# Kernel tuning notes

Measured on AMD Instinct MI355X. Metric: run time of the kernel, lower is better.

Reference implementation:

```python
import jax, jax.numpy as jnp
import numpy as np
import math

IN_DIM = 256
HID_DIM = 256
NUM_EDGE_TYPES = 3
HEADS = 8
HEAD_DIM = HID_DIM // HEADS  # 32
QK_DIM = (NUM_EDGE_TYPES + 1) * HID_DIM  # 1024
N = 4096


def _glorot(key, shape):
    # torch_geometric-style glorot: uniform(-a, a), a = sqrt(6/(fan_in+fan_out)) over last two dims
    a = math.sqrt(6.0 / (shape[-2] + shape[-1]))
    return jax.random.uniform(key, shape, jnp.float32, -a, a)


def setup_inputs() -> dict:
    key = jax.random.key(0)
    ks = jax.random.split(key, 8)
    return {
        "input_x": jax.random.normal(ks[0], (N, IN_DIM), jnp.float32),
        "pe_Q": jax.random.normal(ks[1], (N, NUM_EDGE_TYPES * HID_DIM), jnp.float32),
        "pe_K": jax.random.normal(ks[2], (N, NUM_EDGE_TYPES * HID_DIM), jnp.float32),
        "A": jnp.zeros((N, N), jnp.int32),  # accepted by forward but unused
        "WQ": _glorot(ks[3], (HEADS, QK_DIM, HEAD_DIM)),
        "WK": _glorot(ks[4], (HEADS, QK_DIM, HEAD_DIM)),
        "WV": _glorot(ks[5], (HEADS, IN_DIM, HEAD_DIM)),
        "Q_bias": jnp.zeros((HEADS, 1, HEAD_DIM), jnp.float32),
        "K_bias": jnp.zeros((HEADS, 1, HEAD_DIM), jnp.float32),
        "V_bias": jnp.zeros((HEADS, 1, HEAD_DIM), jnp.float32),
        "lin_w": _glorot(ks[6], (HID_DIM, HID_DIM)),
        "lin_b": jnp.zeros((HID_DIM,), jnp.float32),
    }


def reference(input_x, pe_Q, pe_K, A, WQ, WK, WV, Q_bias, K_bias, V_bias, lin_w, lin_b):
    x_Q = jnp.concatenate([input_x, pe_Q], axis=-1)  # [N, QK_DIM]
    x_K = jnp.concatenate([input_x, pe_K], axis=-1)  # [N, QK_DIM]
    Q = jnp.einsum('nd,hdk->hnk', x_Q, WQ) + Q_bias   # [H, N, hd]
    K = jnp.einsum('nd,hdk->hnk', x_K, WK) + K_bias   # [H, N, hd]
    V = jnp.einsum('nd,hdk->hnk', input_x, WV) + V_bias
    scores = jnp.einsum('hnk,hmk->hnm', Q, K) / math.sqrt(HID_DIM)  # [H, N, N]
    scores = scores - jax.lax.stop_gradient(jnp.max(scores, axis=-1, keepdims=True))
    attn = jax.nn.softmax(scores, axis=-1)
    attn = jnp.where(jnp.isnan(attn), jnp.zeros_like(attn), attn)
    attn_x = jnp.einsum('hnm,hmk->hnk', attn, V)      # [H, N, hd]
    # cat(list over heads, dim=1) -> [N, H*hd] with head-major column order
    x_cat = jnp.transpose(attn_x, (1, 0, 2)).reshape(attn_x.shape[1], -1)
    return x_cat @ lin_w.T + lin_b
```

## Files before the change

kernel.cpp:

```cpp
#include <hip/hip_runtime.h>
#include <hip/hip_bf16.h>

typedef __attribute__((ext_vector_type(8))) short bf16x8;
typedef __attribute__((ext_vector_type(4))) float f32x4;

#define QSCALE 0.09016844f

__device__ __forceinline__ unsigned short f2b(float f) {
    union { float f; unsigned int u; } v; v.f = f;
    unsigned int u = v.u;
    unsigned int r = (u + 0x7FFFu + ((u >> 16) & 1u)) >> 16;
    return (unsigned short)r;
}
__device__ __forceinline__ float b2f(unsigned short h) {
    union { unsigned int u; float f; } v; v.u = ((unsigned int)h) << 16;
    return v.f;
}
__device__ __forceinline__ unsigned pk2(float a, float b) {
    union { __hip_bfloat162 h; unsigned u; } c;
    c.h = __float22bfloat162_rn(make_float2(a, b));
    return c.u;
}

__global__ __launch_bounds__(256) void prep_main(
    const float* __restrict__ WQ, const float* __restrict__ WK,
    const float* __restrict__ WV, const float* __restrict__ LW,
    const float* __restrict__ Qb, const float* __restrict__ Kb,
    const float* __restrict__ Vb,
    const float* __restrict__ x, const float* __restrict__ peQ,
    const float* __restrict__ peK,
    unsigned short* __restrict__ WQt, unsigned short* __restrict__ WKt,
    unsigned short* __restrict__ WVt, unsigned short* __restrict__ LWt,
    unsigned short* __restrict__ Bq, unsigned short* __restrict__ Bk,
    unsigned short* __restrict__ Bv,
    unsigned short* __restrict__ xb, unsigned short* __restrict__ peQb,
    unsigned short* __restrict__ peKb) {
    int b = blockIdx.x, t = threadIdx.x;
    if (b < 288) {
        const float* W; unsigned short* Wt; int h, d0, D; float sc = 1.0f;
        if (b < 128)      { W = WQ; Wt = WQt; h = b >> 4;   d0 = (b & 15) * 64; D = 1024; sc = QSCALE; }
        else if (b < 256) { int bb = b - 128; W = WK; Wt = WKt; h = bb >> 4; d0 = (bb & 15) * 64; D = 1024; }
        else              { int bb = b - 256; W = WV; Wt = WVt; h = bb >> 2; d0 = (bb & 3) * 64;  D = 256; }
        __shared__ float Ts[32][65];
        int dr = t >> 2, k0 = (t & 3) * 8;
        const float* src = W + (h * D + d0 + dr) * 32 + k0;
        float4 u0 = *(const float4*)src;
        float4 u1 = *(const float4*)(src + 4);
        Ts[k0 + 0][dr] = u0.x; Ts[k0 + 1][dr] = u0.y; Ts[k0 + 2][dr] = u0.z; Ts[k0 + 3][dr] = u0.w;
        Ts[k0 + 4][dr] = u1.x; Ts[k0 + 5][dr] = u1.y; Ts[k0 + 6][dr] = u1.z; Ts[k0 + 7][dr] = u1.w;
        __syncthreads();
        int k = t >> 3, dc = (t & 7) * 8;
        union { unsigned short s[8]; uint4 v; } pk;
#pragma unroll
        for (int i = 0; i < 8; i++) pk.s[i] = f2b(Ts[k][dc + i] * sc);
        *(uint4*)(Wt + (h * 32 + k) * D + d0 + dc) = pk.v;
    } else if (b < 320) {
        int base = (b - 288) * 2048 + t * 8;
        const float* sp = LW + base;
        float4 u0 = *(const float4*)sp;
        float4 u1 = *(const float4*)(sp + 4);
        union { unsigned u[4]; uint4 v; } pk;
        pk.u[0] = pk2(u0.x, u0.y); pk.u[1] = pk2(u0.z, u0.w);
        pk.u[2] = pk2(u1.x, u1.y); pk.u[3] = pk2(u1.z, u1.w);
        *(uint4*)(LWt + base) = pk.v;
    } else if (b == 320) {
        Bq[t] = f2b(Qb[t] * QSCALE); Bk[t] = f2b(Kb[t]); Bv[t] = f2b(Vb[t]);
    } else {
        int idx = (b - 321) * 2048 + t * 8;
        const float* sp; unsigned short* dp;
        if (idx < 1048576)      { sp = x + idx;                dp = xb + idx; }
        else if (idx < 4194304) { sp = peQ + (idx - 1048576);  dp = peQb + (idx - 1048576); }
        else                    { sp = peK + (idx - 4194304);  dp = peKb + (idx - 4194304); }
        float4 u0 = *(const float4*)sp;
        float4 u1 = *(const float4*)(sp + 4);
        union { unsigned u[4]; uint4 v; } pk;
        pk.u[0] = pk2(u0.x, u0.y); pk.u[1] = pk2(u0.z, u0.w);
        pk.u[2] = pk2(u1.x, u1.y); pk.u[3] = pk2(u1.z, u1.w);
        *(uint4*)dp = pk.v;
    }
}

__global__ __launch_bounds__(256) void prep_fb(
    const float* __restrict__ WQ, const float* __restrict__ WK,
    const float* __restrict__ WV,
    const float* __restrict__ Qb, const float* __restrict__ Kb,
    const float* __restrict__ Vb,
    unsigned short* __restrict__ WQt, unsigned short* __restrict__ WKt,
    unsigned short* __restrict__ WVt,
    unsigned short* __restrict__ Bq, unsigned short* __restrict__ Bk,
    unsigned short* __restrict__ Bv) {
    int b = blockIdx.x, t = threadIdx.x;
    if (b < 288) {
        const float* W; unsigned short* Wt; int h, d0, D; float sc = 1.0f;
        if (b < 128)      { W = WQ; Wt = WQt; h = b >> 4;   d0 = (b & 15) * 64; D = 1024; sc = QSCALE; }
        else if (b < 256) { int bb = b - 128; W = WK; Wt = WKt; h = bb >> 4; d0 = (bb & 15) * 64; D = 1024; }
        else              { int bb = b - 256; W = WV; Wt = WVt; h = bb >> 2; d0 = (bb & 3) * 64;  D = 256; }
        __shared__ float Ts[32][65];
        int dr = t >> 2, k0 = (t & 3) * 8;
        const float* src = W + (h * D + d0 + dr) * 32 + k0;
        float4 u0 = *(const float4*)src;
        float4 u1 = *(const float4*)(src + 4);
        Ts[k0 + 0][dr] = u0.x; Ts[k0 + 1][dr] = u0.y; Ts[k0 + 2][dr] = u0.z; Ts[k0 + 3][dr] = u0.w;
        Ts[k0 + 4][dr] = u1.x; Ts[k0 + 5][dr] = u1.y; Ts[k0 + 6][dr] = u1.z; Ts[k0 + 7][dr] = u1.w;
        __syncthreads();
        int k = t >> 3, dc = (t & 7) * 8;
        union { unsigned short s[8]; uint4 v; } pk;
#pragma unroll
        for (int i = 0; i < 8; i++) pk.s[i] = f2b(Ts[k][dc + i] * sc);
        *(uint4*)(Wt + (h * 32 + k) * D + d0 + dc) = pk.v;
    } else {
        Bq[t] = f2b(Qb[t] * QSCALE); Bk[t] = f2b(Kb[t]); Bv[t] = f2b(Vb[t]);
    }
}

template <bool ABF16>
__global__ __launch_bounds__(256) void proj_fused(
    const void* __restrict__ xv,
    const void* __restrict__ peQv, const void* __restrict__ peKv,
    const unsigned short* __restrict__ WQt, const unsigned short* __restrict__ WKt,
    const unsigned short* __restrict__ WVt,
    const unsigned short* __restrict__ Bq, const unsigned short* __restrict__ Bk,
    const unsigned short* __restrict__ Bv,
    unsigned short* __restrict__ Qc, unsigned short* __restrict__ KV) {
    __shared__ unsigned short As[64 * 72];
    __shared__ unsigned short Bs[64 * 72];
    int bx = blockIdx.x;
    int which = bx >> 8, bb = bx & 255;
    const void* A1; const unsigned short* Bt; const unsigned short* bias; int K;
    if (which == 0)      { A1 = peQv; Bt = WQt; bias = Bq; K = 1024; }
    else if (which == 1) { A1 = peKv; Bt = WKt; bias = Bk; K = 1024; }
    else                 { A1 = peQv; Bt = WVt; bias = Bv; K = 256; }
    int mb = bb & 63, nb = bb >> 6;
    int m0 = mb * 64, n0 = nb * 64;
    int t = threadIdx.x, w = t >> 6, lane = t & 63;
    int ln = lane & 15, q8 = (lane >> 4) * 8;
    int wm = (w >> 1) * 32, wn = (w & 1) * 32;
    int sr = t >> 3, sc = (t & 7) * 8;
    f32x4 acc[2][2];
#pragma unroll
    for (int i = 0; i < 2; i++)
#pragma unroll
        for (int j = 0; j < 2; j++) acc[i][j] = (f32x4){0.f, 0.f, 0.f, 0.f};
    for (int kb = 0; kb < K; kb += 64) {
#pragma unroll
        for (int half = 0; half < 2; half++) {
            int r = sr + half * 32;
            int c = kb + sc;
            if (ABF16) {
                const unsigned short* ap = (c < 256)
                    ? ((const unsigned short*)xv + (m0 + r) * 256 + c)
                    : ((const unsigned short*)A1 + (m0 + r) * 768 + (c - 256));
                *(uint4*)&As[r * 72 + sc] = *(const uint4*)ap;
            } else {
                const float* ap = (c < 256)
                    ? ((const float*)xv + (m0 + r) * 256 + c)
                    : ((const float*)A1 + (m0 + r) * 768 + (c - 256));
                float4 u0 = *(const float4*)ap;
                float4 u1 = *(const float4*)(ap + 4);
                union { unsigned u[4]; uint4 v; } pk;
                pk.u[0] = pk2(u0.x, u0.y); pk.u[1] = pk2(u0.z, u0.w);
                pk.u[2] = pk2(u1.x, u1.y); pk.u[3] = pk2(u1.z, u1.w);
                *(uint4*)&As[r * 72 + sc] = pk.v;
            }
            *(uint4*)&Bs[r * 72 + sc] = *(const uint4*)(Bt + (n0 + r) * K + c);
        }
        __syncthreads();
#pragma unroll
        for (int ks = 0; ks < 64; ks += 32) {
            bf16x8 a[2], b[2];
#pragma unroll
            for (int i = 0; i < 2; i++) {
                a[i] = *(const bf16x8*)&As[(wm + i * 16 + ln) * 72 + ks + q8];
                b[i] = *(const bf16x8*)&Bs[(wn + i * 16 + ln) * 72 + ks + q8];
            }
#pragma unroll
            for (int i = 0; i < 2; i++)
#pragma unroll
                for (int j = 0; j < 2; j++)
                    acc[i][j] = __builtin_amdgcn_mfma_f32_16x16x32_bf16(a[i], b[j], acc[i][j], 0, 0, 0);
        }
        __syncthreads();
    }
#pragma unroll
    for (int j = 0; j < 2; j++) {
        int ncol = n0 + wn + j * 16 + ln;
        float bv = b2f(bias[ncol]);
        int h2 = ncol >> 5, din = ncol & 31;
#pragma unroll
        for (int i = 0; i < 2; i++) {
            int rbase = m0 + wm + i * 16 + ((lane >> 4) * 4);
            if (which == 0) {
#pragma unroll
                for (int r = 0; r < 4; r++)
                    Qc[(rbase + r) * 256 + ncol] = f2b(acc[i][j][r] + bv);
            } else if (which == 1) {
#pragma unroll
                for (int r = 0; r < 4; r++) {
                    int key = rbase + r;
                    int T2 = key >> 6, k6 = key & 63;
                    int kt = ((k6 >> 2) & 1) + ((k6 >> 4) & 2);
                    int ln2 = ((k6 >> 3) & 3) * 4 + (k6 & 3);
                    int addr = (h2 * 64 + T2) * 4096 + kt * 512
                             + ((din >> 3) * 16 + ln2) * 8 + (din & 7);
                    KV[addr] = f2b(acc[i][j][r] + bv);
                }
            } else {
                int key = rbase;
                int T2 = key >> 6, k6 = key & 63;
                int chunk = 4 + ((din >> 4) << 1) + ((k6 >> 5) & 1);
                int lane2 = ((k6 >> 3) & 3) * 16 + (din & 15);
                int addr = (h2 * 64 + T2) * 4096 + chunk * 512 + lane2 * 8 + (k6 & 7);
                uint2 vv;
                vv.x = pk2(acc[i][j][0] + bv, acc[i][j][1] + bv);
                vv.y = pk2(acc[i][j][2] + bv, acc[i][j][3] + bv);
                *(uint2*)(KV + addr) = vv;
            }
        }
    }
}

__global__ __launch_bounds__(512, 4) void attn_kernel(
    const unsigned short* __restrict__ Qc,
    const unsigned short* __restrict__ KV,
    unsigned short* __restrict__ Xc) {
    __shared__ float Om[8][32][33];
    __shared__ float Ls[8][32];
    int head = blockIdx.x & 7;
    int qb = blockIdx.x >> 3;
    int t = threadIdx.x, w = t >> 6, lane = t & 63;
    int ln = lane & 15, quad = lane >> 4, q8 = quad * 8;
    int wq = w >> 2, wk = w & 3;
    int q0 = qb * 64;
    bf16x8 qfv[2];
#pragma unroll
    for (int qf = 0; qf < 2; qf++)
        qfv[qf] = *(const bf16x8*)(Qc + (q0 + wq * 32 + qf * 16 + ln) * 256 + head * 32 + q8);
    const unsigned short* kv = KV + (head * 64 + wk * 16) * 4096 + lane * 8;
    f32x4 o[2][2];
    float lts[2] = {0.f, 0.f};
#pragma unroll
    for (int qf = 0; qf < 2; qf++)
#pragma unroll
        for (int hh = 0; hh < 2; hh++) o[qf][hh] = (f32x4){0.f, 0.f, 0.f, 0.f};
    const f32x4 z = {0.f, 0.f, 0.f, 0.f};
    bf16x8 k0 = *(const bf16x8*)(kv + 0);
    bf16x8 k1 = *(const bf16x8*)(kv + 512);
    bf16x8 k2 = *(const bf16x8*)(kv + 1024);
    bf16x8 k3 = *(const bf16x8*)(kv + 1536);
    bf16x8 v0 = *(const bf16x8*)(kv + 2048);
    bf16x8 v1 = *(const bf16x8*)(kv + 2560);
    bf16x8 v2 = *(const bf16x8*)(kv + 3072);
    bf16x8 v3 = *(const bf16x8*)(kv + 3584);
#pragma unroll 1
    for (int it = 0; it < 16; it++) {
        int nit = (it < 15) ? (it + 1) : 15;
        const unsigned short* nkv = kv + nit * 4096;
        bf16x8 nk0 = *(const bf16x8*)(nkv + 0);
        bf16x8 nk1 = *(const bf16x8*)(nkv + 512);
        bf16x8 nk2 = *(const bf16x8*)(nkv + 1024);
        bf16x8 nk3 = *(const bf16x8*)(nkv + 1536);
        bf16x8 nv0 = *(const bf16x8*)(nkv + 2048);
        bf16x8 nv1 = *(const bf16x8*)(nkv + 2560);
        bf16x8 nv2 = *(const bf16x8*)(nkv + 3072);
        bf16x8 nv3 = *(const bf16x8*)(nkv + 3584);
#pragma unroll
        for (int qf = 0; qf < 2; qf++) {
            f32x4 s0 = __builtin_amdgcn_mfma_f32_16x16x32_bf16(k0, qfv[qf], z, 0, 0, 0);
            f32x4 s1 = __builtin_amdgcn_mfma_f32_16x16x32_bf16(k1, qfv[qf], z, 0, 0, 0);
            f32x4 s2 = __builtin_amdgcn_mfma_f32_16x16x32_bf16(k2, qfv[qf], z, 0, 0, 0);
            f32x4 s3 = __builtin_amdgcn_mfma_f32_16x16x32_bf16(k3, qfv[qf], z, 0, 0, 0);
            float p0[4], p1[4], p2[4], p3[4];
#pragma unroll
            for (int r = 0; r < 4; r++) {
                p0[r] = __builtin_amdgcn_exp2f(s0[r]);
                p1[r] = __builtin_amdgcn_exp2f(s1[r]);
                p2[r] = __builtin_amdgcn_exp2f(s2[r]);
                p3[r] = __builtin_amdgcn_exp2f(s3[r]);
            }
            float psum = 0.f;
#pragma unroll
            for (int r = 0; r < 4; r++) psum += (p0[r] + p1[r]) + (p2[r] + p3[r]);
            lts[qf] += psum;
            union { unsigned u[4]; bf16x8 v; } b0, b1;
            b0.u[0] = pk2(p0[0], p0[1]); b0.u[1] = pk2(p0[2], p0[3]);
            b0.u[2] = pk2(p1[0], p1[1]); b0.u[3] = pk2(p1[2], p1[3]);
            b1.u[0] = pk2(p2[0], p2[1]); b1.u[1] = pk2(p2[2], p2[3]);
            b1.u[2] = pk2(p3[0], p3[1]); b1.u[3] = pk2(p3[2], p3[3]);
            o[qf][0] = __builtin_amdgcn_mfma_f32_16x16x32_bf16(v0, b0.v, o[qf][0], 0, 0, 0);
            o[qf][0] = __builtin_amdgcn_mfma_f32_16x16x32_bf16(v1, b1.v, o[qf][0], 0, 0, 0);
            o[qf][1] = __builtin_amdgcn_mfma_f32_16x16x32_bf16(v2, b0.v, o[qf][1], 0, 0, 0);
            o[qf][1] = __builtin_amdgcn_mfma_f32_16x16x32_bf16(v3, b1.v, o[qf][1], 0, 0, 0);
        }
        k0 = nk0; k1 = nk1; k2 = nk2; k3 = nk3;
        v0 = nv0; v1 = nv1; v2 = nv2; v3 = nv3;
    }
#pragma unroll
    for (int qf = 0; qf < 2; qf++) {
        float l = lts[qf];
        l += __shfl_xor(l, 16, 64);
        l += __shfl_xor(l, 32, 64);
#pragma unroll
        for (int r = 0; r < 4; r++) {
            Om[w][quad * 4 + r][qf * 16 + ln] = o[qf][0][r];
            Om[w][16 + quad * 4 + r][qf * 16 + ln] = o[qf][1][r];
        }
        if (quad == 0) Ls[w][qf * 16 + ln] = l;
    }
    __syncthreads();
    int q6 = t & 63, d = (t >> 6) * 4;
    int g = q6 >> 5, ql = q6 & 31;
    float num[4] = {0.f, 0.f, 0.f, 0.f};
    float den = 0.f;
#pragma unroll
    for (int w2 = 0; w2 < 4; w2++) {
        int ws2 = g * 4 + w2;
        den += Ls[ws2][ql];
#pragma unroll
        for (int i = 0; i < 4; i++) num[i] += Om[ws2][d + i][ql];
    }
    float inv = 1.f / den;
    uint2 outv;
    outv.x = pk2(num[0] * inv, num[1] * inv);
    outv.y = pk2(num[2] * inv, num[3] * inv);
    *(uint2*)(Xc + (q0 + q6) * 256 + head * 32 + d) = outv;
}

template <bool BBF16>
__global__ __launch_bounds__(256) void gemm_out(
    const unsigned short* __restrict__ A,
    const void* __restrict__ LWv,
    const float* __restrict__ Lb,
    float* __restrict__ C) {
    __shared__ unsigned short As[64 * 72];
    __shared__ unsigned short Bs[64 * 72];
    int mb = blockIdx.x & 63, nb = blockIdx.x >> 6;
    int m0 = mb * 64, n0 = nb * 64;
    int t = threadIdx.x, w = t >> 6, lane = t & 63;
    int ln = lane & 15, q8 = (lane >> 4) * 8;
    int wm = (w >> 1) * 32, wn = (w & 1) * 32;
    int sr = t >> 3, sc = (t & 7) * 8;
    f32x4 acc[2][2];
#pragma unroll
    for (int i = 0; i < 2; i++)
#pragma unroll
        for (int j = 0; j < 2; j++) acc[i][j] = (f32x4){0.f, 0.f, 0.f, 0.f};
    for (int kb = 0; kb < 256; kb += 64) {
#pragma unroll
        for (int half = 0; half < 2; half++) {
            int r = sr + half * 32;
            int c = kb + sc;
            *(uint4*)&As[r * 72 + sc] = *(const uint4*)(A + (m0 + r) * 256 + c);
            if (BBF16) {
                *(uint4*)&Bs[r * 72 + sc] =
                    *(const uint4*)((const unsigned short*)LWv + (n0 + r) * 256 + c);
            } else {
                const float* bp = (const float*)LWv + (n0 + r) * 256 + c;
                float4 u0 = *(const float4*)bp;
                float4 u1 = *(const float4*)(bp + 4);
                union { unsigned u[4]; uint4 v; } pk;
                pk.u[0] = pk2(u0.x, u0.y); pk.u[1] = pk2(u0.z, u0.w);
                pk.u[2] = pk2(u1.x, u1.y); pk.u[3] = pk2(u1.z, u1.w);
                *(uint4*)&Bs[r * 72 + sc] = pk.v;
            }
        }
        __syncthreads();
#pragma unroll
        for (int ks = 0; ks < 64; ks += 32) {
            bf16x8 a[2], b[2];
#pragma unroll
            for (int i = 0; i < 2; i++) {
                a[i] = *(const bf16x8*)&As[(wm + i * 16 + ln) * 72 + ks + q8];
                b[i] = *(const bf16x8*)&Bs[(wn + i * 16 + ln) * 72 + ks + q8];
            }
#pragma unroll
            for (int i = 0; i < 2; i++)
#pragma unroll
                for (int j = 0; j < 2; j++)
                    acc[i][j] = __builtin_amdgcn_mfma_f32_16x16x32_bf16(a[i], b[j], acc[i][j], 0, 0, 0);
        }
        __syncthreads();
    }
#pragma unroll
    for (int j = 0; j < 2; j++) {
        int ncol = n0 + wn + j * 16 + ln;
        float bv = Lb[ncol];
#pragma unroll
        for (int i = 0; i < 2; i++) {
            int rbase = m0 + wm + i * 16 + ((lane >> 4) * 4);
#pragma unroll
            for (int r = 0; r < 4; r++)
                C[(rbase + r) * 256 + ncol] = acc[i][j][r] + bv;
        }
    }
}

extern "C" void kernel_launch(void* const* d_in, const int* in_sizes, int n_in,
                              void* d_out, int out_size, void* d_ws, size_t ws_size,
                              hipStream_t stream) {
    const float* input_x = (const float*)d_in[0];
    const float* pe_Q    = (const float*)d_in[1];
    const float* pe_K    = (const float*)d_in[2];
    const float* WQ = (const float*)d_in[4];
    const float* WK = (const float*)d_in[5];
    const float* WV = (const float*)d_in[6];
    const float* Qb = (const float*)d_in[7];
    const float* Kb = (const float*)d_in[8];
    const float* Vb = (const float*)d_in[9];
    const float* lw = (const float*)d_in[10];
    const float* lb = (const float*)d_in[11];
    float* outp = (float*)d_out;

    unsigned short* ws = (unsigned short*)d_ws;
    unsigned short* WQt = ws;
    unsigned short* WKt = WQt + 262144;
    unsigned short* WVt = WKt + 262144;
    unsigned short* LWt = WVt + 65536;
    unsigned short* Bq  = LWt + 65536;
    unsigned short* Bk  = Bq + 256;
    unsigned short* Bv  = Bk + 256;
    unsigned short* xb   = Bv + 256;
    unsigned short* peQb = xb + 1048576;
    unsigned short* peKb = peQb + 3145728;
    unsigned short* Qc   = peKb + 3145728;
    unsigned short* KVb  = Qc + 1048576;
    unsigned short* Xc   = KVb + 2097152;
    size_t need = (size_t)(Xc + 1048576 - ws) * 2;

    if (ws_size >= need) {
        prep_main<<<dim3(3905), dim3(256), 0, stream>>>(
            WQ, WK, WV, lw, Qb, Kb, Vb, input_x, pe_Q, pe_K,
            WQt, WKt, WVt, LWt, Bq, Bk, Bv, xb, peQb, peKb);
        proj_fused<true><<<dim3(768), dim3(256), 0, stream>>>(
            xb, peQb, peKb, WQt, WKt, WVt, Bq, Bk, Bv, Qc, KVb);
        attn_kernel<<<dim3(512), dim3(512), 0, stream>>>(Qc, KVb, Xc);
        gemm_out<true><<<dim3(256), dim3(256), 0, stream>>>(Xc, LWt, lb, outp);
    } else {
        unsigned short* Qc2  = Bv + 256;
        unsigned short* KV2  = Qc2 + 1048576;
        unsigned short* Xc2  = KV2 + 2097152;
        prep_fb<<<dim3(289), dim3(256), 0, stream>>>(WQ, WK, WV, Qb, Kb, Vb,
                                                     WQt, WKt, WVt, Bq, Bk, Bv);
        proj_fused<false><<<dim3(768), dim3(256), 0, stream>>>(
            input_x, pe_Q, pe_K, WQt, WKt, WVt, Bq, Bk, Bv, Qc2, KV2);
        attn_kernel<<<dim3(512), dim3(512), 0, stream>>>(Qc2, KV2, Xc2);
        gemm_out<false><<<dim3(256), dim3(256), 0, stream>>>(Xc2, lw, lb, outp);
    }
}
```

Before: 177.1 us.

## Fuse activation bf16 conversion into projection and widen attention key split

Removes the separate pass that converted input_x, pe_Q and pe_K to bf16 in workspace. The projection GEMM now loads fp32 activations and converts them while staging into shared memory, which avoids an extra write and reread of about 14M elements. The attention kernel is also restructured so each of the 8 waves handles all 64 queries over a disjoint eighth of the keys, instead of a 2x4 query/key split. This doubles Q-fragment reuse per loaded K/V and halves loop iterations, at the cost of more registers (launch bounds lowered to 2) and a larger shared-memory reduction.

```diff
diff --git a/kernel.cpp b/kernel.cpp
--- a/kernel.cpp
+++ b/kernel.cpp
@@ -27,66 +27,8 @@
     const float* __restrict__ WV, const float* __restrict__ LW,
     const float* __restrict__ Qb, const float* __restrict__ Kb,
     const float* __restrict__ Vb,
-    const float* __restrict__ x, const float* __restrict__ peQ,
-    const float* __restrict__ peK,
     unsigned short* __restrict__ WQt, unsigned short* __restrict__ WKt,
     unsigned short* __restrict__ WVt, unsigned short* __restrict__ LWt,
-    unsigned short* __restrict__ Bq, unsigned short* __restrict__ Bk,
-    unsigned short* __restrict__ Bv,
-    unsigned short* __restrict__ xb, unsigned short* __restrict__ peQb,
-    unsigned short* __restrict__ peKb) {
-    int b = blockIdx.x, t = threadIdx.x;
-    if (b < 288) {
-        const float* W; unsigned short* Wt; int h, d0, D; float sc = 1.0f;
-        if (b < 128)      { W = WQ; Wt = WQt; h = b >> 4;   d0 = (b & 15) * 64; D = 1024; sc = QSCALE; }
-        else if (b < 256) { int bb = b - 128; W = WK; Wt = WKt; h = bb >> 4; d0 = (bb & 15) * 64; D = 1024; }
-        else              { int bb = b - 256; W = WV; Wt = WVt; h = bb >> 2; d0 = (bb & 3) * 64;  D = 256; }
-        __shared__ float Ts[32][65];
-        int dr = t >> 2, k0 = (t & 3) * 8;
-        const float* src = W + (h * D + d0 + dr) * 32 + k0;
-        float4 u0 = *(const float4*)src;
-        float4 u1 = *(const float4*)(src + 4);
-        Ts[k0 + 0][dr] = u0.x; Ts[k0 + 1][dr] = u0.y; Ts[k0 + 2][dr] = u0.z; Ts[k0 + 3][dr] = u0.w;
-        Ts[k0 + 4][dr] = u1.x; Ts[k0 + 5][dr] = u1.y; Ts[k0 + 6][dr] = u1.z; Ts[k0 + 7][dr] = u1.w;
-        __syncthreads();
-        int k = t >> 3, dc = (t & 7) * 8;
-        union { unsigned short s[8]; uint4 v; } pk;
-#pragma unroll
-        for (int i = 0; i < 8; i++) pk.s[i] = f2b(Ts[k][dc + i] * sc);
-        *(uint4*)(Wt + (h * 32 + k) * D + d0 + dc) = pk.v;
-    } else if (b < 320) {
-        int base = (b - 288) * 2048 + t * 8;
-        const float* sp = LW + base;
-        float4 u0 = *(const float4*)sp;
-        float4 u1 = *(const float4*)(sp + 4);
-        union { unsigned u[4]; uint4 v; } pk;
-        pk.u[0] = pk2(u0.x, u0.y); pk.u[1] = pk2(u0.z, u0.w);
-        pk.u[2] = pk2(u1.x, u1.y); pk.u[3] = pk2(u1.z, u1.w);
-        *(uint4*)(LWt + base) = pk.v;
-    } else if (b == 320) {
-        Bq[t] = f2b(Qb[t] * QSCALE); Bk[t] = f2b(Kb[t]); Bv[t] = f2b(Vb[t]);
-    } else {
-        int idx = (b - 321) * 2048 + t * 8;
-        const float* sp; unsigned short* dp;
-        if (idx < 1048576)      { sp = x + idx;                dp = xb + idx; }
-        else if (idx < 4194304) { sp = peQ + (idx - 1048576);  dp = peQb + (idx - 1048576); }
-        else                    { sp = peK + (idx - 4194304);  dp = peKb + (idx - 4194304); }
-        float4 u0 = *(const float4*)sp;
-        float4 u1 = *(const float4*)(sp + 4);
-        union { unsigned u[4]; uint4 v; } pk;
-        pk.u[0] = pk2(u0.x, u0.y); pk.u[1] = pk2(u0.z, u0.w);
-        pk.u[2] = pk2(u1.x, u1.y); pk.u[3] = pk2(u1.z, u1.w);
-        *(uint4*)dp = pk.v;
-    }
-}
-
-__global__ __launch_bounds__(256) void prep_fb(
-    const float* __restrict__ WQ, const float* __restrict__ WK,
-    const float* __restrict__ WV,
-    const float* __restrict__ Qb, const float* __restrict__ Kb,
-    const float* __restrict__ Vb,
-    unsigned short* __restrict__ WQt, unsigned short* __restrict__ WKt,
-    unsigned short* __restrict__ WVt,
     unsigned short* __restrict__ Bq, unsigned short* __restrict__ Bk,
     unsigned short* __restrict__ Bv) {
     int b = blockIdx.x, t = threadIdx.x;
@@ -108,15 +50,23 @@
 #pragma unroll
         for (int i = 0; i < 8; i++) pk.s[i] = f2b(Ts[k][dc + i] * sc);
         *(uint4*)(Wt + (h * 32 + k) * D + d0 + dc) = pk.v;
+    } else if (b < 320) {
+        int base = (b - 288) * 2048 + t * 8;
+        const float* sp = LW + base;
+        float4 u0 = *(const float4*)sp;
+        float4 u1 = *(const float4*)(sp + 4);
+        union { unsigned u[4]; uint4 v; } pk;
+        pk.u[0] = pk2(u0.x, u0.y); pk.u[1] = pk2(u0.z, u0.w);
+        pk.u[2] = pk2(u1.x, u1.y); pk.u[3] = pk2(u1.z, u1.w);
+        *(uint4*)(LWt + base) = pk.v;
     } else {
         Bq[t] = f2b(Qb[t] * QSCALE); Bk[t] = f2b(Kb[t]); Bv[t] = f2b(Vb[t]);
     }
 }
 
-template <bool ABF16>
 __global__ __launch_bounds__(256) void proj_fused(
-    const void* __restrict__ xv,
-    const void* __restrict__ peQv, const void* __restrict__ peKv,
+    const float* __restrict__ xv,
+    const float* __restrict__ peQv, const float* __restrict__ peKv,
     const unsigned short* __restrict__ WQt, const unsigned short* __restrict__ WKt,
     const unsigned short* __restrict__ WVt,
     const unsigned short* __restrict__ Bq, const unsigned short* __restrict__ Bk,
@@ -126,7 +76,7 @@
     __shared__ unsigned short Bs[64 * 72];
     int bx = blockIdx.x;
     int which = bx >> 8, bb = bx & 255;
-    const void* A1; const unsigned short* Bt; const unsigned short* bias; int K;
+    const float* A1; const unsigned short* Bt; const unsigned short* bias; int K;
     if (which == 0)      { A1 = peQv; Bt = WQt; bias = Bq; K = 1024; }
     else if (which == 1) { A1 = peKv; Bt = WKt; bias = Bk; K = 1024; }
     else                 { A1 = peQv; Bt = WVt; bias = Bv; K = 256; }
@@ -146,22 +96,15 @@
         for (int half = 0; half < 2; half++) {
             int r = sr + half * 32;
             int c = kb + sc;
-            if (ABF16) {
-                const unsigned short* ap = (c < 256)
-                    ? ((const unsigned short*)xv + (m0 + r) * 256 + c)
-                    : ((const unsigned short*)A1 + (m0 + r) * 768 + (c - 256));
-                *(uint4*)&As[r * 72 + sc] = *(const uint4*)ap;
-            } else {
-                const float* ap = (c < 256)
-                    ? ((const float*)xv + (m0 + r) * 256 + c)
-                    : ((const float*)A1 + (m0 + r) * 768 + (c - 256));
-                float4 u0 = *(const float4*)ap;
-                float4 u1 = *(const float4*)(ap + 4);
-                union { unsigned u[4]; uint4 v; } pk;
-                pk.u[0] = pk2(u0.x, u0.y); pk.u[1] = pk2(u0.z, u0.w);
-                pk.u[2] = pk2(u1.x, u1.y); pk.u[3] = pk2(u1.z, u1.w);
-                *(uint4*)&As[r * 72 + sc] = pk.v;
-            }
+            const float* ap = (c < 256)
+                ? (xv + (m0 + r) * 256 + c)
+                : (A1 + (m0 + r) * 768 + (c - 256));
+            float4 u0 = *(const float4*)ap;
+            float4 u1 = *(const float4*)(ap + 4);
+            union { unsigned u[4]; uint4 v; } pk;
+            pk.u[0] = pk2(u0.x, u0.y); pk.u[1] = pk2(u0.z, u0.w);
+            pk.u[2] = pk2(u1.x, u1.y); pk.u[3] = pk2(u1.z, u1.w);
+            *(uint4*)&As[r * 72 + sc] = pk.v;
             *(uint4*)&Bs[r * 72 + sc] = *(const uint4*)(Bt + (n0 + r) * K + c);
         }
         __syncthreads();
@@ -219,27 +162,26 @@
     }
 }
 
-__global__ __launch_bounds__(512, 4) void attn_kernel(
+__global__ __launch_bounds__(512, 2) void attn_kernel(
     const unsigned short* __restrict__ Qc,
     const unsigned short* __restrict__ KV,
     unsigned short* __restrict__ Xc) {
-    __shared__ float Om[8][32][33];
-    __shared__ float Ls[8][32];
+    __shared__ float Om[8][32][65];
+    __shared__ float Ls[8][64];
     int head = blockIdx.x & 7;
     int qb = blockIdx.x >> 3;
     int t = threadIdx.x, w = t >> 6, lane = t & 63;
     int ln = lane & 15, quad = lane >> 4, q8 = quad * 8;
-    int wq = w >> 2, wk = w & 3;
     int q0 = qb * 64;
-    bf16x8 qfv[2];
-#pragma unroll
-    for (int qf = 0; qf < 2; qf++)
-        qfv[qf] = *(const bf16x8*)(Qc + (q0 + wq * 32 + qf * 16 + ln) * 256 + head * 32 + q8);
-    const unsigned short* kv = KV + (head * 64 + wk * 16) * 4096 + lane * 8;
-    f32x4 o[2][2];
-    float lts[2] = {0.f, 0.f};
-#pragma unroll
-    for (int qf = 0; qf < 2; qf++)
+    bf16x8 qfv[4];
+#pragma unroll
+    for (int qf = 0; qf < 4; qf++)
+        qfv[qf] = *(const bf16x8*)(Qc + (q0 + qf * 16 + ln) * 256 + head * 32 + q8);
+    const unsigned short* kv = KV + (head * 64 + w * 8) * 4096 + lane * 8;
+    f32x4 o[4][2];
+    float lts[4] = {0.f, 0.f, 0.f, 0.f};
+#pragma unroll
+    for (int qf = 0; qf < 4; qf++)
 #pragma unroll
         for (int hh = 0; hh < 2; hh++) o[qf][hh] = (f32x4){0.f, 0.f, 0.f, 0.f};
     const f32x4 z = {0.f, 0.f, 0.f, 0.f};
@@ -252,8 +194,8 @@
     bf16x8 v2 = *(const bf16x8*)(kv + 3072);
     bf16x8 v3 = *(const bf16x8*)(kv + 3584);
 #pragma unroll 1
-    for (int it = 0; it < 16; it++) {
-        int nit = (it < 15) ? (it + 1) : 15;
+    for (int it = 0; it < 8; it++) {
+        int nit = (it < 7) ? (it + 1) : 7;
         const unsigned short* nkv = kv + nit * 4096;
         bf16x8 nk0 = *(const bf16x8*)(nkv + 0);
         bf16x8 nk1 = *(const bf16x8*)(nkv + 512);
@@ -264,7 +206,7 @@
         bf16x8 nv2 = *(const bf16x8*)(nkv + 3072);
         bf16x8 nv3 = *(const bf16x8*)(nkv + 3584);
 #pragma unroll
-        for (int qf = 0; qf < 2; qf++) {
+        for (int qf = 0; qf < 4; qf++) {
             f32x4 s0 = __builtin_amdgcn_mfma_f32_16x16x32_bf16(k0, qfv[qf], z, 0, 0, 0);
             f32x4 s1 = __builtin_amdgcn_mfma_f32_16x16x32_bf16(k1, qfv[qf], z, 0, 0, 0);
             f32x4 s2 = __builtin_amdgcn_mfma_f32_16x16x32_bf16(k2, qfv[qf], z, 0, 0, 0);
@@ -295,7 +237,7 @@
         v0 = nv0; v1 = nv1; v2 = nv2; v3 = nv3;
     }
 #pragma unroll
-    for (int qf = 0; qf < 2; qf++) {
+    for (int qf = 0; qf < 4; qf++) {
         float l = lts[qf];
         l += __shfl_xor(l, 16, 64);
         l += __shfl_xor(l, 32, 64);
@@ -308,15 +250,13 @@
     }
     __syncthreads();
     int q6 = t & 63, d = (t >> 6) * 4;
-    int g = q6 >> 5, ql = q6 & 31;
     float num[4] = {0.f, 0.f, 0.f, 0.f};
     float den = 0.f;
 #pragma unroll
-    for (int w2 = 0; w2 < 4; w2++) {
-        int ws2 = g * 4 + w2;
-        den += Ls[ws2][ql];
-#pragma unroll
-        for (int i = 0; i < 4; i++) num[i] += Om[ws2][d + i][ql];
+    for (int w2 = 0; w2 < 8; w2++) {
+        den += Ls[w2][q6];
+#pragma unroll
+        for (int i = 0; i < 4; i++) num[i] += Om[w2][d + i][q6];
     }
     float inv = 1.f / den;
     uint2 outv;
@@ -325,10 +265,9 @@
     *(uint2*)(Xc + (q0 + q6) * 256 + head * 32 + d) = outv;
 }
 
-template <bool BBF16>
 __global__ __launch_bounds__(256) void gemm_out(
     const unsigned short* __restrict__ A,
-    const void* __restrict__ LWv,
+    const unsigned short* __restrict__ LWt,
     const float* __restrict__ Lb,
     float* __restrict__ C) {
     __shared__ unsigned short As[64 * 72];
@@ -350,18 +289,7 @@
             int r = sr + half * 32;
             int c = kb + sc;
             *(uint4*)&As[r * 72 + sc] = *(const uint4*)(A + (m0 + r) * 256 + c);
-            if (BBF16) {
-                *(uint4*)&Bs[r * 72 + sc] =
-                    *(const uint4*)((const unsigned short*)LWv + (n0 + r) * 256 + c);
-            } else {
-                const float* bp = (const float*)LWv + (n0 + r) * 256 + c;
-                float4 u0 = *(const float4*)bp;
-                float4 u1 = *(const float4*)(bp + 4);
-                union { unsigned u[4]; uint4 v; } pk;
-                pk.u[0] = pk2(u0.x, u0.y); pk.u[1] = pk2(u0.z, u0.w);
-                pk.u[2] = pk2(u1.x, u1.y); pk.u[3] = pk2(u1.z, u1.w);
-                *(uint4*)&Bs[r * 72 + sc] = pk.v;
-            }
+            *(uint4*)&Bs[r * 72 + sc] = *(const uint4*)(LWt + (n0 + r) * 256 + c);
         }
         __syncthreads();
 #pragma unroll
@@ -418,31 +346,15 @@
     unsigned short* Bq  = LWt + 65536;
     unsigned short* Bk  = Bq + 256;
     unsigned short* Bv  = Bk + 256;
-    unsigned short* xb   = Bv + 256;
-    unsigned short* peQb = xb + 1048576;
-    unsigned short* peKb = peQb + 3145728;
-    unsigned short* Qc   = peKb + 3145728;
-    unsigned short* KVb  = Qc + 1048576;
-    unsigned short* Xc   = KVb + 2097152;
-    size_t need = (size_t)(Xc + 1048576 - ws) * 2;
-
-    if (ws_size >= need) {
-        prep_main<<<dim3(3905), dim3(256), 0, stream>>>(
-            WQ, WK, WV, lw, Qb, Kb, Vb, input_x, pe_Q, pe_K,
-            WQt, WKt, WVt, LWt, Bq, Bk, Bv, xb, peQb, peKb);
-        proj_fused<true><<<dim3(768), dim3(256), 0, stream>>>(
-            xb, peQb, peKb, WQt, WKt, WVt, Bq, Bk, Bv, Qc, KVb);
-        attn_kernel<<<dim3(512), dim3(512), 0, stream>>>(Qc, KVb, Xc);
-        gemm_out<true><<<dim3(256), dim3(256), 0, stream>>>(Xc, LWt, lb, outp);
-    } else {
-        unsigned short* Qc2  = Bv + 256;
-        unsigned short* KV2  = Qc2 + 1048576;
-        unsigned short* Xc2  = KV2 + 2097152;
-        prep_fb<<<dim3(289), dim3(256), 0, stream>>>(WQ, WK, WV, Qb, Kb, Vb,
-                                                     WQt, WKt, WVt, Bq, Bk, Bv);
-        proj_fused<false><<<dim3(768), dim3(256), 0, stream>>>(
-            input_x, pe_Q, pe_K, WQt, WKt, WVt, Bq, Bk, Bv, Qc2, KV2);
-        attn_kernel<<<dim3(512), dim3(512), 0, stream>>>(Qc2, KV2, Xc2);
-        gemm_out<false><<<dim3(256), dim3(256), 0, stream>>>(Xc2, lw, lb, outp);
-    }
-}
+    unsigned short* Qc  = Bv + 256;
+    unsigned short* KVb = Qc + 1048576;
+    unsigned short* Xc  = KVb + 2097152;
+
+    prep_main<<<dim3(321), dim3(256), 0, stream>>>(
+        WQ, WK, WV, lw, Qb, Kb, Vb,
+        WQt, WKt, WVt, LWt, Bq, Bk, Bv);
+    proj_fused<<<dim3(768), dim3(256), 0, stream>>>(
+        input_x, pe_Q, pe_K, WQt, WKt, WVt, Bq, Bk, Bv, Qc, KVb);
+    attn_kernel<<<dim3(512), dim3(512), 0, stream>>>(Qc, KVb, Xc);
+    gemm_out<<<dim3(256), dim3(256), 0, stream>>>(Xc, LWt, lb, outp);
+}
```

Result: slower. 183.2 us (+3.4%).
